# Kernel tuning notes

Hardware: AMD Instinct MI355X
Metric: run time of the kernel (lower is better)

The kernel has to match this reference:

```python
import jax, jax.numpy as jnp
import numpy as np

N_NODES = 100000
N_EDGES = 1200000
N_GRAPHS = 1024
IN_FEATS = 64
HID = 64
BN_EPS = 1e-5


def setup_inputs() -> dict:
    key = jax.random.key(0)
    ks = jax.random.split(key, 20)
    feats = jax.random.normal(ks[0], (N_NODES, IN_FEATS), jnp.float32)
    src = jax.random.randint(ks[1], (N_EDGES,), 0, N_NODES, jnp.int32)
    dst = jax.random.randint(ks[2], (N_EDGES,), 0, N_NODES, jnp.int32)
    graph_ids = jnp.sort(jax.random.randint(ks[3], (N_NODES,), 0, N_GRAPHS, jnp.int32))

    def lin(k, fi, fo):
        s = 1.0 / np.sqrt(fi)
        kw, kb = jax.random.split(k)
        return (jax.random.uniform(kw, (fi, fo), jnp.float32, -s, s),
                jax.random.uniform(kb, (fo,), jnp.float32, -s, s))

    W_self, _ = lin(ks[4], IN_FEATS, HID)
    W_neigh, b_neigh = lin(ks[5], IN_FEATS, HID)
    W1, b1 = lin(ks[6], HID, 128)
    W2, b2 = lin(ks[7], 128, 64)
    W3, b3 = lin(ks[8], 64, 1)

    def bn(k, d):
        k1, k2, k3, k4 = jax.random.split(k, 4)
        return (jax.random.normal(k1, (d,), jnp.float32) * 0.1 + 1.0,
                jax.random.normal(k2, (d,), jnp.float32) * 0.1,
                jax.random.normal(k3, (d,), jnp.float32) * 0.1,
                jax.random.uniform(k4, (d,), jnp.float32, 0.5, 1.5))

    g1, be1, rm1, rv1 = bn(ks[9], 128)
    g2, be2, rm2, rv2 = bn(ks[10], 64)

    return dict(feats=feats, src=src, dst=dst, graph_ids=graph_ids,
                W_self=W_self, W_neigh=W_neigh, b_neigh=b_neigh,
                W1=W1, b1=b1, g1=g1, be1=be1, rm1=rm1, rv1=rv1,
                W2=W2, b2=b2, g2=g2, be2=be2, rm2=rm2, rv2=rv2,
                W3=W3, b3=b3)


def reference(feats, src, dst, graph_ids, W_self, W_neigh, b_neigh,
              W1, b1, g1, be1, rm1, rv1, W2, b2, g2, be2, rm2, rv2, W3, b3):
    # --- SAGEConv (mean aggregator): h = W_self@h_self + W_neigh@mean_neigh + b
    deg = jax.ops.segment_sum(jnp.ones((src.shape[0],), feats.dtype), dst,
                              num_segments=N_NODES)                      # [N]
    agg = jax.ops.segment_sum(feats[src], dst, num_segments=N_NODES)     # [N, F]
    mean_neigh = agg / jnp.maximum(deg, 1.0)[:, None]
    h = feats @ W_self + mean_neigh @ W_neigh + b_neigh
    h = jax.nn.relu(h)                                                   # activation

    # --- per-graph max readout (dgl.max_nodes)
    hg = jax.ops.segment_max(h, graph_ids, num_segments=N_GRAPHS)        # [G, HID]

    # --- MLP head with eval-mode BatchNorm1d
    def bn(x, g, b, rm, rv):
        return (x - rm) * jax.lax.rsqrt(rv + BN_EPS) * g + b

    x = bn(jax.nn.relu(hg @ W1 + b1), g1, be1, rm1, rv1)
    x = bn(jax.nn.relu(x @ W2 + b2), g2, be2, rm2, rv2)
    return x @ W3 + b3                                                   # [G, n_task]
```

## Files before the change

### kernel.cpp

```cpp
#include <hip/hip_runtime.h>
#include <hip/hip_fp16.h>

#define N_NODES  100000
#define N_EDGES  1200000
#define N_GRAPHS 1024
#define F        64
#define BN_EPS   1e-5f
#define NBUCK    ((N_NODES + 255) / 256)
#define NBLK     256
#define CHUNK    ((N_EDGES + NBLK - 1) / NBLK)
#define MT       128
#define GEMM_BLOCKS ((N_NODES + MT - 1) / MT)
#define CE       3584

typedef _Float16 f16x8 __attribute__((ext_vector_type(8)));
typedef float f32x4 __attribute__((ext_vector_type(4)));

__global__ __launch_bounds__(256) void prepw(
    const float* __restrict__ Wself, const float* __restrict__ Wneigh,
    __half* __restrict__ Wh) {
  int t = threadIdx.x;
  for (int i = t; i < 128 * 64; i += 256) {
    int c = i >> 6, k = i & 63;
    float v = (c < 64) ? Wself[k * 64 + c] : Wneigh[k * 64 + (c - 64)];
    Wh[i] = __float2half_rn(v);
  }
}

__global__ __launch_bounds__(256) void prepscat(
    const float* __restrict__ feats, const __half* __restrict__ Wh,
    __half* __restrict__ Uh, __half* __restrict__ Zh,
    const int* __restrict__ src, const int* __restrict__ dst,
    int* __restrict__ gcur, int* __restrict__ pairs) {
  __shared__ int lh[NBUCK];
  __shared__ int lcur[NBUCK];
  int t = threadIdx.x;

  if (blockIdx.x >= GEMM_BLOCKS) {
    int b = blockIdx.x - GEMM_BLOCKS;
    for (int i = t; i < NBUCK; i += 256) lh[i] = 0;
    __syncthreads();
    int e0 = b * CHUNK, e1 = e0 + CHUNK;
    if (e1 > N_EDGES) e1 = N_EDGES;
    for (int e = e0 + t; e < e1; e += 256) atomicAdd(&lh[dst[e] >> 8], 1);
    __syncthreads();
    for (int i = t; i < NBUCK; i += 256) {
      int c = lh[i];
      lcur[i] = c ? atomicAdd(&gcur[i], c) : 0;
    }
    __syncthreads();
    for (int e = e0 + t; e < e1; e += 256) {
      int d = dst[e];
      int pos = atomicAdd(&lcur[d >> 8], 1);
      if (pos < CE)
        pairs[(size_t)(d >> 8) * CE + pos] =
            (int)((((unsigned)d & 255u) << 24) | (unsigned)src[e]);
    }
    return;
  }

  int mbase = blockIdx.x * MT;
  int wave = t >> 6, lane = t & 63;
  int lr = lane & 15, kg = lane >> 4;
  int r0 = wave * 32;

  int n0 = mbase + r0 + lr;
  int n1 = n0 + 16;
  int n0c = (n0 < N_NODES) ? n0 : (N_NODES - 1);
  int n1c = (n1 < N_NODES) ? n1 : (N_NODES - 1);
  const float* fp0 = feats + (size_t)n0c * F + kg * 8;
  const float* fp1 = feats + (size_t)n1c * F + kg * 8;

  f16x8 a0[2], a1[2];
#pragma unroll
  for (int h = 0; h < 2; h++) {
    float4 x0 = *(const float4*)(fp0 + h * 32);
    float4 x1 = *(const float4*)(fp0 + h * 32 + 4);
    float4 y0 = *(const float4*)(fp1 + h * 32);
    float4 y1 = *(const float4*)(fp1 + h * 32 + 4);
    a0[h] = (f16x8){(_Float16)x0.x, (_Float16)x0.y, (_Float16)x0.z, (_Float16)x0.w,
                    (_Float16)x1.x, (_Float16)x1.y, (_Float16)x1.z, (_Float16)x1.w};
    a1[h] = (f16x8){(_Float16)y0.x, (_Float16)y0.y, (_Float16)y0.z, (_Float16)y0.w,
                    (_Float16)y1.x, (_Float16)y1.y, (_Float16)y1.z, (_Float16)y1.w};
  }

  f32x4 acc[2][8];
#pragma unroll
  for (int i = 0; i < 2; i++)
#pragma unroll
    for (int j = 0; j < 8; j++) acc[i][j] = (f32x4){0.f, 0.f, 0.f, 0.f};

  const __half* wp = Wh + (size_t)lr * 64 + kg * 8;
#pragma unroll
  for (int h = 0; h < 2; h++) {
#pragma unroll
    for (int j = 0; j < 8; j++) {
      f16x8 wv = *(const f16x8*)(wp + j * 16 * 64 + h * 32);
      acc[0][j] = __builtin_amdgcn_mfma_f32_16x16x32_f16(wv, a0[h], acc[0][j], 0, 0, 0);
      acc[1][j] = __builtin_amdgcn_mfma_f32_16x16x32_f16(wv, a1[h], acc[1][j], 0, 0, 0);
    }
  }

#pragma unroll
  for (int i = 0; i < 2; i++) {
    int node = mbase + r0 + i * 16 + lr;
    if (node < N_NODES) {
#pragma unroll
      for (int j = 0; j < 8; j++) {
        int f = j * 16 + kg * 4;
        union { __half h[4]; uint2 u; } pk;
        pk.h[0] = __float2half_rn(acc[i][j][0]);
        pk.h[1] = __float2half_rn(acc[i][j][1]);
        pk.h[2] = __float2half_rn(acc[i][j][2]);
        pk.h[3] = __float2half_rn(acc[i][j][3]);
        __half* outp = (f < 64) ? (Uh + (size_t)node * F + f)
                                : (Zh + (size_t)node * F + (f - 64));
        *(uint2*)outp = pk.u;
      }
    }
  }
}

__global__ __launch_bounds__(1024) void gather_place(
    const __half* __restrict__ Uh, const __half* __restrict__ Zh,
    const int* __restrict__ pairs, const int* __restrict__ gcur,
    const float* __restrict__ bneigh, const int* __restrict__ gids,
    int* __restrict__ hgbits) {
  __shared__ int eidx_l[CE];
  __shared__ int rsl[256];
  __shared__ int lh[256];
  __shared__ int cur[256];
  int b = blockIdx.x, t = threadIdx.x;
  int nb0 = b << 8;
  const int* pr = pairs + (size_t)b * CE;
  int E = gcur[b]; if (E > CE) E = CE;

  if (t < 256) lh[t] = 0;
  __syncthreads();
  for (int e = t; e < E; e += 1024)
    atomicAdd(&lh[((unsigned)pr[e]) >> 24], 1);
  __syncthreads();
  if (t < 256) cur[t] = lh[t];
  __syncthreads();
  for (int off = 1; off < 256; off <<= 1) {
    int u = (t < 256 && t >= off) ? cur[t - off] : 0;
    __syncthreads();
    if (t < 256) cur[t] += u;
    __syncthreads();
  }
  if (t < 256) { int ex = cur[t] - lh[t]; rsl[t] = ex; cur[t] = ex; }
  __syncthreads();
  for (int e = t; e < E; e += 1024) {
    unsigned p = (unsigned)pr[e];
    int pos = atomicAdd(&cur[p >> 24], 1);
    eidx_l[pos] = (int)(p & 0xFFFFFFu);
  }
  __syncthreads();

  int wave = t >> 6, lane = t & 63;
  int fl = lane & 15, sub = lane >> 4;
  float4 b4 = *(const float4*)(bneigh + 4 * fl);
  int nl = wave * 16;
  int nend = nl + 16;
  if (nb0 + nl >= N_NODES) return;
  if (nb0 + nend > N_NODES) nend = N_NODES - nb0;

  int curg = gids[nb0 + nl];
  float4 gmax = {0.f, 0.f, 0.f, 0.f};

  for (; nl < nend; nl++) {
    int node = nb0 + nl;
    int rr  = rsl[nl];
    int deg = lh[nl];
    uint2 ur = *(const uint2*)(Uh + (size_t)node * F + 4 * fl);
    float sx = 0.f, sy = 0.f, sz = 0.f, sw = 0.f;
    for (int jj = 0; jj < deg; jj += 16) {
      int j0 = jj + sub;
      int s0 = (j0      < deg) ? eidx_l[rr + j0]      : 0;
      int s1 = (j0 + 4  < deg) ? eidx_l[rr + j0 + 4]  : 0;
      int s2 = (j0 + 8  < deg) ? eidx_l[rr + j0 + 8]  : 0;
      int s3 = (j0 + 12 < deg) ? eidx_l[rr + j0 + 12] : 0;
      uint2 z0 = *(const uint2*)(Zh + (size_t)s0 * F + 4 * fl);
      uint2 z1 = *(const uint2*)(Zh + (size_t)s1 * F + 4 * fl);
      uint2 z2 = *(const uint2*)(Zh + (size_t)s2 * F + 4 * fl);
      uint2 z3 = *(const uint2*)(Zh + (size_t)s3 * F + 4 * fl);
      if (j0 < deg) {
        float2 f0 = __half22float2(*(__half2*)&z0.x);
        float2 f1 = __half22float2(*(__half2*)&z0.y);
        sx += f0.x; sy += f0.y; sz += f1.x; sw += f1.y;
      }
      if (j0 + 4 < deg) {
        float2 f0 = __half22float2(*(__half2*)&z1.x);
        float2 f1 = __half22float2(*(__half2*)&z1.y);
        sx += f0.x; sy += f0.y; sz += f1.x; sw += f1.y;
      }
      if (j0 + 8 < deg) {
        float2 f0 = __half22float2(*(__half2*)&z2.x);
        float2 f1 = __half22float2(*(__half2*)&z2.y);
        sx += f0.x; sy += f0.y; sz += f1.x; sw += f1.y;
      }
      if (j0 + 12 < deg) {
        float2 f0 = __half22float2(*(__half2*)&z3.x);
        float2 f1 = __half22float2(*(__half2*)&z3.y);
        sx += f0.x; sy += f0.y; sz += f1.x; sw += f1.y;
      }
    }
    sx += __shfl_xor(sx, 16); sy += __shfl_xor(sy, 16);
    sz += __shfl_xor(sz, 16); sw += __shfl_xor(sw, 16);
    sx += __shfl_xor(sx, 32); sy += __shfl_xor(sy, 32);
    sz += __shfl_xor(sz, 32); sw += __shfl_xor(sw, 32);
    float inv = 1.0f / fmaxf((float)deg, 1.0f);

    int g = gids[node];
    if (g != curg) {
      if (sub == 0) {
        int* hp = hgbits + (size_t)curg * F + 4 * fl;
        atomicMax(hp + 0, __float_as_int(gmax.x));
        atomicMax(hp + 1, __float_as_int(gmax.y));
        atomicMax(hp + 2, __float_as_int(gmax.z));
        atomicMax(hp + 3, __float_as_int(gmax.w));
      }
      curg = g; gmax = make_float4(0.f, 0.f, 0.f, 0.f);
    }

    float2 uf0 = __half22float2(*(__half2*)&ur.x);
    float2 uf1 = __half22float2(*(__half2*)&ur.y);
    gmax.x = fmaxf(gmax.x, fmaxf(uf0.x + sx * inv + b4.x, 0.f));
    gmax.y = fmaxf(gmax.y, fmaxf(uf0.y + sy * inv + b4.y, 0.f));
    gmax.z = fmaxf(gmax.z, fmaxf(uf1.x + sz * inv + b4.z, 0.f));
    gmax.w = fmaxf(gmax.w, fmaxf(uf1.y + sw * inv + b4.w, 0.f));
  }
  if (sub == 0) {
    int* hp = hgbits + (size_t)curg * F + 4 * fl;
    atomicMax(hp + 0, __float_as_int(gmax.x));
    atomicMax(hp + 1, __float_as_int(gmax.y));
    atomicMax(hp + 2, __float_as_int(gmax.z));
    atomicMax(hp + 3, __float_as_int(gmax.w));
  }
}

#define GPB 2
__global__ __launch_bounds__(128) void mlp(
    const float* __restrict__ hg,
    const float* __restrict__ W1, const float* __restrict__ b1,
    const float* __restrict__ g1, const float* __restrict__ be1,
    const float* __restrict__ rm1, const float* __restrict__ rv1,
    const float* __restrict__ W2, const float* __restrict__ b2,
    const float* __restrict__ g2, const float* __restrict__ be2,
    const float* __restrict__ rm2, const float* __restrict__ rv2,
    const float* __restrict__ W3, const float* __restrict__ b3,
    float* __restrict__ out) {
  __shared__ float W1s[64 * 128];
  __shared__ float W2s[128 * 64];
  __shared__ float W3s[64];
  __shared__ float sc1[128], sh1[128], b1s[128];
  __shared__ float sc2[64],  sh2[64],  b2s[64];
  __shared__ float s0[64], s1[128], s2[64];
  int t = threadIdx.x;

  for (int i = t; i < 64 * 128; i += 128) W1s[i] = W1[i];
  for (int i = t; i < 128 * 64; i += 128) W2s[i] = W2[i];
  if (t < 64) W3s[t] = W3[t];
  {
    float iv = rsqrtf(rv1[t] + BN_EPS);
    float sc = g1[t] * iv;
    sc1[t] = sc; sh1[t] = be1[t] - rm1[t] * sc; b1s[t] = b1[t];
  }
  if (t < 64) {
    float iv = rsqrtf(rv2[t] + BN_EPS);
    float sc = g2[t] * iv;
    sc2[t] = sc; sh2[t] = be2[t] - rm2[t] * sc; b2s[t] = b2[t];
  }
  __syncthreads();

  for (int gg = 0; gg < GPB; gg++) {
    int g = blockIdx.x * GPB + gg;
    if (t < 64) s0[t] = hg[(size_t)g * F + t];
    __syncthreads();
    {
      float acc = b1s[t];
      for (int i = 0; i < 64; i++) acc += s0[i] * W1s[i * 128 + t];
      acc = fmaxf(acc, 0.0f);
      s1[t] = acc * sc1[t] + sh1[t];
    }
    __syncthreads();
    if (t < 64) {
      float acc = b2s[t];
      for (int i = 0; i < 128; i++) acc += s1[i] * W2s[i * 64 + t];
      acc = fmaxf(acc, 0.0f);
      s2[t] = acc * sc2[t] + sh2[t];
    }
    __syncthreads();
    if (t < 64) {
      float p = s2[t] * W3s[t];
      for (int off = 32; off > 0; off >>= 1) p += __shfl_down(p, off);
      if (t == 0) out[g] = p + b3[0];
    }
    __syncthreads();
  }
}

extern "C" void kernel_launch(void* const* d_in, const int* in_sizes, int n_in,
                              void* d_out, int out_size, void* d_ws, size_t ws_size,
                              hipStream_t stream) {
  const float* feats  = (const float*)d_in[0];
  const int*   src    = (const int*)d_in[1];
  const int*   dst    = (const int*)d_in[2];
  const int*   gids   = (const int*)d_in[3];
  const float* Wself  = (const float*)d_in[4];
  const float* Wneigh = (const float*)d_in[5];
  const float* bneigh = (const float*)d_in[6];
  const float* W1  = (const float*)d_in[7];
  const float* b1  = (const float*)d_in[8];
  const float* g1  = (const float*)d_in[9];
  const float* be1 = (const float*)d_in[10];
  const float* rm1 = (const float*)d_in[11];
  const float* rv1 = (const float*)d_in[12];
  const float* W2  = (const float*)d_in[13];
  const float* b2  = (const float*)d_in[14];
  const float* g2  = (const float*)d_in[15];
  const float* be2 = (const float*)d_in[16];
  const float* rm2 = (const float*)d_in[17];
  const float* rv2 = (const float*)d_in[18];
  const float* W3  = (const float*)d_in[19];
  const float* b3  = (const float*)d_in[20];

  __half* Uh   = (__half*)d_ws;
  __half* Zh   = Uh + (size_t)N_NODES * F;
  __half* Wh   = Zh + (size_t)N_NODES * F;
  int* gcur    = (int*)(Wh + 128 * 64);
  int* hgbits  = gcur + NBUCK;
  int* pairs   = hgbits + (size_t)N_GRAPHS * F;

  hipMemsetAsync(gcur, 0, (NBUCK + N_GRAPHS * F) * sizeof(int), stream);

  prepw<<<1, 256, 0, stream>>>(Wself, Wneigh, Wh);
  prepscat<<<GEMM_BLOCKS + NBLK, 256, 0, stream>>>(feats, Wh, Uh, Zh,
                                                   src, dst, gcur, pairs);
  gather_place<<<NBUCK, 1024, 0, stream>>>(Uh, Zh, pairs, gcur, bneigh,
                                           gids, hgbits);
  mlp<<<N_GRAPHS / GPB, 128, 0, stream>>>((const float*)hgbits,
                                          W1, b1, g1, be1, rm1, rv1,
                                          W2, b2, g2, be2, rm2, rv2, W3, b3,
                                          (float*)d_out);
}
```

Before: 201.2 us.

## Vectorize edge bucketing, schedule scatter blocks first, halve GEMM tile

```diff
diff --git a/kernel.cpp b/kernel.cpp
--- a/kernel.cpp
+++ b/kernel.cpp
@@ -7,9 +7,9 @@
 #define F        64
 #define BN_EPS   1e-5f
 #define NBUCK    ((N_NODES + 255) / 256)
-#define NBLK     256
+#define NBLK     512
 #define CHUNK    ((N_EDGES + NBLK - 1) / NBLK)
-#define MT       128
+#define MT       64
 #define GEMM_BLOCKS ((N_NODES + MT - 1) / MT)
 #define CE       3584
 
@@ -36,59 +36,82 @@
   __shared__ int lcur[NBUCK];
   int t = threadIdx.x;
 
-  if (blockIdx.x >= GEMM_BLOCKS) {
-    int b = blockIdx.x - GEMM_BLOCKS;
+  if (blockIdx.x < NBLK) {
+    int b = blockIdx.x;
     for (int i = t; i < NBUCK; i += 256) lh[i] = 0;
     __syncthreads();
-    int e0 = b * CHUNK, e1 = e0 + CHUNK;
-    if (e1 > N_EDGES) e1 = N_EDGES;
-    for (int e = e0 + t; e < e1; e += 256) atomicAdd(&lh[dst[e] >> 8], 1);
+    int e0 = b * CHUNK;
+    int e1 = e0 + CHUNK; if (e1 > N_EDGES) e1 = N_EDGES;
+    for (int q = t; q < CHUNK / 4; q += 256) {
+      int e = e0 + q * 4;
+      if (e + 4 <= e1) {
+        int4 dv = *(const int4*)(dst + e);
+        atomicAdd(&lh[dv.x >> 8], 1);
+        atomicAdd(&lh[dv.y >> 8], 1);
+        atomicAdd(&lh[dv.z >> 8], 1);
+        atomicAdd(&lh[dv.w >> 8], 1);
+      } else {
+        for (int k = 0; k < 4; k++)
+          if (e + k < e1) atomicAdd(&lh[dst[e + k] >> 8], 1);
+      }
+    }
     __syncthreads();
     for (int i = t; i < NBUCK; i += 256) {
       int c = lh[i];
       lcur[i] = c ? atomicAdd(&gcur[i], c) : 0;
     }
     __syncthreads();
-    for (int e = e0 + t; e < e1; e += 256) {
-      int d = dst[e];
-      int pos = atomicAdd(&lcur[d >> 8], 1);
-      if (pos < CE)
-        pairs[(size_t)(d >> 8) * CE + pos] =
-            (int)((((unsigned)d & 255u) << 24) | (unsigned)src[e]);
+    for (int q = t; q < CHUNK / 4; q += 256) {
+      int e = e0 + q * 4;
+      if (e + 4 <= e1) {
+        int4 dv = *(const int4*)(dst + e);
+        int4 sv = *(const int4*)(src + e);
+        int p0 = atomicAdd(&lcur[dv.x >> 8], 1);
+        int p1 = atomicAdd(&lcur[dv.y >> 8], 1);
+        int p2 = atomicAdd(&lcur[dv.z >> 8], 1);
+        int p3 = atomicAdd(&lcur[dv.w >> 8], 1);
+        if (p0 < CE) pairs[(size_t)(dv.x >> 8) * CE + p0] =
+            (int)((((unsigned)dv.x & 255u) << 24) | (unsigned)sv.x);
+        if (p1 < CE) pairs[(size_t)(dv.y >> 8) * CE + p1] =
+            (int)((((unsigned)dv.y & 255u) << 24) | (unsigned)sv.y);
+        if (p2 < CE) pairs[(size_t)(dv.z >> 8) * CE + p2] =
+            (int)((((unsigned)dv.z & 255u) << 24) | (unsigned)sv.z);
+        if (p3 < CE) pairs[(size_t)(dv.w >> 8) * CE + p3] =
+            (int)((((unsigned)dv.w & 255u) << 24) | (unsigned)sv.w);
+      } else {
+        for (int k = 0; k < 4; k++)
+          if (e + k < e1) {
+            int d = dst[e + k];
+            int pos = atomicAdd(&lcur[d >> 8], 1);
+            if (pos < CE)
+              pairs[(size_t)(d >> 8) * CE + pos] =
+                  (int)((((unsigned)d & 255u) << 24) | (unsigned)src[e + k]);
+          }
+      }
     }
     return;
   }
 
-  int mbase = blockIdx.x * MT;
+  int mbase = (blockIdx.x - NBLK) * MT;
   int wave = t >> 6, lane = t & 63;
   int lr = lane & 15, kg = lane >> 4;
-  int r0 = wave * 32;
-
-  int n0 = mbase + r0 + lr;
-  int n1 = n0 + 16;
+
+  int n0 = mbase + wave * 16 + lr;
   int n0c = (n0 < N_NODES) ? n0 : (N_NODES - 1);
-  int n1c = (n1 < N_NODES) ? n1 : (N_NODES - 1);
-  const float* fp0 = feats + (size_t)n0c * F + kg * 8;
-  const float* fp1 = feats + (size_t)n1c * F + kg * 8;
-
-  f16x8 a0[2], a1[2];
+  const float* fp = feats + (size_t)n0c * F + kg * 8;
+
+  f16x8 a[2];
 #pragma unroll
   for (int h = 0; h < 2; h++) {
-    float4 x0 = *(const float4*)(fp0 + h * 32);
-    float4 x1 = *(const float4*)(fp0 + h * 32 + 4);
-    float4 y0 = *(const float4*)(fp1 + h * 32);
-    float4 y1 = *(const float4*)(fp1 + h * 32 + 4);
-    a0[h] = (f16x8){(_Float16)x0.x, (_Float16)x0.y, (_Float16)x0.z, (_Float16)x0.w,
-                    (_Float16)x1.x, (_Float16)x1.y, (_Float16)x1.z, (_Float16)x1.w};
-    a1[h] = (f16x8){(_Float16)y0.x, (_Float16)y0.y, (_Float16)y0.z, (_Float16)y0.w,
-                    (_Float16)y1.x, (_Float16)y1.y, (_Float16)y1.z, (_Float16)y1.w};
-  }
-
-  f32x4 acc[2][8];
-#pragma unroll
-  for (int i = 0; i < 2; i++)
-#pragma unroll
-    for (int j = 0; j < 8; j++) acc[i][j] = (f32x4){0.f, 0.f, 0.f, 0.f};
+    float4 x0 = *(const float4*)(fp + h * 32);
+    float4 x1 = *(const float4*)(fp + h * 32 + 4);
+    a[h] = (f16x8){(_Float16)x0.x, (_Float16)x0.y, (_Float16)x0.z, (_Float16)x0.w,
+                   (_Float16)x1.x, (_Float16)x1.y, (_Float16)x1.z, (_Float16)x1.w};
+  }
+
+  f32x4 acc[8];
+#pragma unroll
+  for (int j = 0; j < 8; j++) acc[j] = (f32x4){0.f, 0.f, 0.f, 0.f};
 
   const __half* wp = Wh + (size_t)lr * 64 + kg * 8;
 #pragma unroll
@@ -96,27 +119,22 @@
 #pragma unroll
     for (int j = 0; j < 8; j++) {
       f16x8 wv = *(const f16x8*)(wp + j * 16 * 64 + h * 32);
-      acc[0][j] = __builtin_amdgcn_mfma_f32_16x16x32_f16(wv, a0[h], acc[0][j], 0, 0, 0);
-      acc[1][j] = __builtin_amdgcn_mfma_f32_16x16x32_f16(wv, a1[h], acc[1][j], 0, 0, 0);
-    }
-  }
-
-#pragma unroll
-  for (int i = 0; i < 2; i++) {
-    int node = mbase + r0 + i * 16 + lr;
-    if (node < N_NODES) {
-#pragma unroll
-      for (int j = 0; j < 8; j++) {
-        int f = j * 16 + kg * 4;
-        union { __half h[4]; uint2 u; } pk;
-        pk.h[0] = __float2half_rn(acc[i][j][0]);
-        pk.h[1] = __float2half_rn(acc[i][j][1]);
-        pk.h[2] = __float2half_rn(acc[i][j][2]);
-        pk.h[3] = __float2half_rn(acc[i][j][3]);
-        __half* outp = (f < 64) ? (Uh + (size_t)node * F + f)
-                                : (Zh + (size_t)node * F + (f - 64));
-        *(uint2*)outp = pk.u;
-      }
+      acc[j] = __builtin_amdgcn_mfma_f32_16x16x32_f16(wv, a[h], acc[j], 0, 0, 0);
+    }
+  }
+
+  if (n0 < N_NODES) {
+#pragma unroll
+    for (int j = 0; j < 8; j++) {
+      int f = j * 16 + kg * 4;
+      union { __half h[4]; uint2 u; } pk;
+      pk.h[0] = __float2half_rn(acc[j][0]);
+      pk.h[1] = __float2half_rn(acc[j][1]);
+      pk.h[2] = __float2half_rn(acc[j][2]);
+      pk.h[3] = __float2half_rn(acc[j][3]);
+      __half* outp = (f < 64) ? (Uh + (size_t)n0 * F + f)
+                              : (Zh + (size_t)n0 * F + (f - 64));
+      *(uint2*)outp = pk.u;
     }
   }
 }
@@ -335,7 +353,7 @@
   hipMemsetAsync(gcur, 0, (NBUCK + N_GRAPHS * F) * sizeof(int), stream);
 
   prepw<<<1, 256, 0, stream>>>(Wself, Wneigh, Wh);
-  prepscat<<<GEMM_BLOCKS + NBLK, 256, 0, stream>>>(feats, Wh, Uh, Zh,
+  prepscat<<<NBLK + GEMM_BLOCKS, 256, 0, stream>>>(feats, Wh, Uh, Zh,
                                                    src, dst, gcur, pairs);
   gather_place<<<NBUCK, 1024, 0, stream>>>(Uh, Zh, pairs, gcur, bneigh,
                                            gids, hgbits);
```

Result: no change. 203.9 us (+1.4%).
